# Kernel optimization log

Measured on AMD Instinct MI355X. Metric: run time of the kernel, lower is better.

## Reference

```python
import jax, jax.numpy as jnp
import numpy as np

N, D, M, K = 65536, 128, 4096, 64

def _xavier_uniform(key, shape):
    fan_out, fan_in = shape
    limit = float(np.sqrt(6.0 / (fan_in + fan_out)))
    return jax.random.uniform(key, shape, jnp.float32, -limit, limit)

def setup_inputs() -> dict:
    key = jax.random.key(0)
    kx, ke, kd = jax.random.split(key, 3)
    x = jax.random.normal(kx, (N, D), jnp.float32)
    W_enc = _xavier_uniform(ke, (M, D))          # [n_latents, input_dim]
    W_dec = _xavier_uniform(kd, (D, M))          # [input_dim, n_latents]
    # normalize decoder columns to unit norm (dim=0), clamped at 1e-8
    norms = jnp.maximum(jnp.linalg.norm(W_dec, axis=0, keepdims=True), 1e-8)
    W_dec = W_dec / norms
    b_enc = jnp.zeros((M,), jnp.float32)
    b_dec = jnp.zeros((D,), jnp.float32)
    return {"x": x, "W_enc": W_enc, "b_enc": b_enc, "W_dec": W_dec, "b_dec": b_dec}

def reference(x, W_enc, b_enc, W_dec, b_dec):
    # encode: z_pre = relu(W_enc @ (x - b_dec) + b_enc)
    z_pre = jax.nn.relu((x - b_dec) @ W_enc.T + b_enc)          # [N, M]
    # TopK activation: keep k largest, zero the rest
    vals, idx = jax.lax.top_k(z_pre, K)                          # [N, K]
    rows = jnp.arange(z_pre.shape[0])[:, None]
    z = jnp.zeros_like(z_pre).at[rows, idx].set(vals)            # sparse [N, M]
    # decode: x_hat = z @ W_dec.T + b_dec
    x_hat = z @ W_dec.T + b_dec                                  # [N, D]
    return (x_hat, z)
```

## Files before the change

kernel.cpp:

```cpp
#include <hip/hip_runtime.h>
#include <cstdint>

#define DDIM 128
#define MLAT 4096
#define KSEL 64

typedef __bf16 bf16x8 __attribute__((ext_vector_type(8)));
typedef float  f32x4  __attribute__((ext_vector_type(4)));

__global__ __launch_bounds__(256) void k_split_x(const float* __restrict__ x,
                                                 const float* __restrict__ bdec,
                                                 ushort* __restrict__ xhi,
                                                 ushort* __restrict__ xlo) {
    int e = (blockIdx.x * 256 + threadIdx.x) * 4;
    float4 v = *(const float4*)(x + e);
    float4 bd = *(const float4*)(bdec + (e & 127));
    float a[4] = {v.x - bd.x, v.y - bd.y, v.z - bd.z, v.w - bd.w};
    ushort4 h, l;
    ushort* hp = (ushort*)&h; ushort* lp = (ushort*)&l;
#pragma unroll
    for (int i = 0; i < 4; ++i) {
        unsigned ua = __float_as_uint(a[i]);
        unsigned rh = (ua + 0x7FFFu + ((ua >> 16) & 1u)) & 0xFFFF0000u;
        float lo = a[i] - __uint_as_float(rh);
        unsigned ul = __float_as_uint(lo);
        unsigned rl = ul + 0x7FFFu + ((ul >> 16) & 1u);
        hp[i] = (ushort)(rh >> 16);
        lp[i] = (ushort)(rl >> 16);
    }
    *(ushort4*)(xhi + e) = h;
    *(ushort4*)(xlo + e) = l;
}

__global__ __launch_bounds__(256) void k_split_w(const float* __restrict__ w,
                                                 ushort* __restrict__ whi,
                                                 ushort* __restrict__ wlo) {
    int e = (blockIdx.x * 256 + threadIdx.x) * 4;
    float4 v = *(const float4*)(w + e);
    float a[4] = {v.x, v.y, v.z, v.w};
    ushort4 h, l;
    ushort* hp = (ushort*)&h; ushort* lp = (ushort*)&l;
#pragma unroll
    for (int i = 0; i < 4; ++i) {
        unsigned ua = __float_as_uint(a[i]);
        unsigned rh = (ua + 0x7FFFu + ((ua >> 16) & 1u)) & 0xFFFF0000u;
        float lo = a[i] - __uint_as_float(rh);
        unsigned ul = __float_as_uint(lo);
        unsigned rl = ul + 0x7FFFu + ((ul >> 16) & 1u);
        hp[i] = (ushort)(rh >> 16);
        lp[i] = (ushort)(rl >> 16);
    }
    *(ushort4*)(whi + e) = h;
    *(ushort4*)(wlo + e) = l;
}

__global__ __launch_bounds__(256) void k_transpose(const float* __restrict__ Wdec,
                                                   float* __restrict__ WdT) {
    int tid = blockIdx.x * 256 + threadIdx.x;
    int d = tid & (DDIM - 1);
    int j = tid >> 7;
    WdT[tid] = Wdec[(size_t)d * MLAT + j];
}

__global__ __launch_bounds__(256, 2) void k_encode_mfma(
        const ushort* __restrict__ xhi, const ushort* __restrict__ xlo,
        const ushort* __restrict__ whi, const ushort* __restrict__ wlo,
        const float* __restrict__ benc, float* __restrict__ zout) {
    __shared__ __attribute__((aligned(16))) ushort Ah[128 * 128];
    __shared__ __attribute__((aligned(16))) ushort Al[128 * 128];

    const int t    = threadIdx.x;
    const int lane = t & 63;
    const int w    = t >> 6;
    const int i0   = blockIdx.x << 7;

    {
        int row = t >> 1, half = t & 1;
        const ushort* sh = xhi + (size_t)(i0 + row) * DDIM + half * 64;
        const ushort* sl = xlo + (size_t)(i0 + row) * DDIM + half * 64;
        int base = row * 256 + half * 128;
        int swz  = (row & 7) << 4;
#pragma unroll
        for (int j = 0; j < 8; ++j) {
            int off = (base + j * 16) ^ swz;
            *(bf16x8*)((char*)Ah + off) = *(const bf16x8*)(sh + j * 8);
            *(bf16x8*)((char*)Al + off) = *(const bf16x8*)(sl + j * 8);
        }
    }
    __syncthreads();

    const int lr = lane & 15;
    const int lq = lane >> 4;

    for (int cp = 0; cp < 16; ++cp) {
        const int jb = cp * 256 + (w << 6);
        f32x4 acc[8][4];
#pragma unroll
        for (int rf = 0; rf < 8; ++rf)
#pragma unroll
            for (int cf = 0; cf < 4; ++cf) acc[rf][cf] = (f32x4){0.f, 0.f, 0.f, 0.f};

        for (int ks = 0; ks < 4; ++ks) {
            bf16x8 bh[4], bl[4];
#pragma unroll
            for (int cf = 0; cf < 4; ++cf) {
                size_t boff = (size_t)(jb + cf * 16 + lr) * DDIM + ks * 32 + lq * 8;
                bh[cf] = *(const bf16x8*)(whi + boff);
                bl[cf] = *(const bf16x8*)(wlo + boff);
            }
#pragma unroll
            for (int rf = 0; rf < 8; ++rf) {
                int row = rf * 16 + lr;
                int off = (row * 256 + ks * 64 + lq * 16) ^ ((row & 7) << 4);
                bf16x8 ah = *(const bf16x8*)((const char*)Ah + off);
                bf16x8 al = *(const bf16x8*)((const char*)Al + off);
#pragma unroll
                for (int cf = 0; cf < 4; ++cf) {
                    acc[rf][cf] = __builtin_amdgcn_mfma_f32_16x16x32_bf16(ah, bh[cf], acc[rf][cf], 0, 0, 0);
                    acc[rf][cf] = __builtin_amdgcn_mfma_f32_16x16x32_bf16(ah, bl[cf], acc[rf][cf], 0, 0, 0);
                    acc[rf][cf] = __builtin_amdgcn_mfma_f32_16x16x32_bf16(al, bh[cf], acc[rf][cf], 0, 0, 0);
                }
            }
        }
#pragma unroll
        for (int rf = 0; rf < 8; ++rf)
#pragma unroll
            for (int cf = 0; cf < 4; ++cf) {
                int col = jb + cf * 16 + lr;
                float be = benc[col];
#pragma unroll
                for (int r = 0; r < 4; ++r) {
                    int row = i0 + rf * 16 + lq * 4 + r;
                    zout[(size_t)row * MLAT + col] = fmaxf(acc[rf][cf][r] + be, 0.f);
                }
            }
    }
}

__global__ __launch_bounds__(128, 8) void k_topk_decode(
        float* __restrict__ zbuf, float* __restrict__ xhat,
        const float* __restrict__ WdT, const float* __restrict__ bdec,
        const float* __restrict__ x, const float* __restrict__ Wenc,
        const float* __restrict__ benc) {
    __shared__ float sval[KSEL];
    __shared__ int   sidx[KSEL];
    __shared__ float bval[128];
    __shared__ int   bidx[128];
    __shared__ unsigned char bselm[128];
    __shared__ unsigned scom[4];
    __shared__ int stot[2];

    const int tid  = threadIdx.x;
    const int lane = tid & 63;
    const int w    = tid >> 6;
    const size_t row = blockIdx.x;
    float* zr = zbuf + row * MLAT;
    const uint4* zu = (const uint4*)zr + (w << 9);

    uint4 u[8];
#pragma unroll
    for (int q = 0; q < 8; ++q) u[q] = zu[(q << 6) + lane];

    unsigned mx = 0u;
#pragma unroll
    for (int q = 0; q < 8; ++q)
        mx = max(mx, max(max(u[q].x, u[q].y), max(u[q].z, u[q].w)));
#pragma unroll
    for (int d = 32; d >= 1; d >>= 1) mx = max(mx, (unsigned)__shfl_xor((int)mx, d, 64));
    if (lane == 0) scom[w] = mx;
    __syncthreads();
    mx = max(scom[0], scom[1]);
    __syncthreads();

#define CNT_GE(T, OUTC)                                              \
    {                                                                \
        int _c = 0;                                                  \
        _Pragma("unroll")                                            \
        for (int q = 0; q < 8; ++q) {                                \
            _c += __popcll(__ballot(u[q].x >= (T)));                 \
            _c += __popcll(__ballot(u[q].y >= (T)));                 \
            _c += __popcll(__ballot(u[q].z >= (T)));                 \
            _c += __popcll(__ballot(u[q].w >= (T)));                 \
        }                                                            \
        if (lane == 0) scom[2 + w] = (unsigned)_c;                   \
        __syncthreads();                                             \
        OUTC = (int)(scom[2] + scom[3]);                             \
        __syncthreads();                                             \
    }

    unsigned T;
    {
        unsigned hi = mx + 1u;
        unsigned lo = (mx > 0x01800000u) ? (mx - 0x01800000u) : 0u;
        int c;
        CNT_GE(lo, c);
        if (c < KSEL) { lo = 0u; c = MLAT; }
        if (c == KSEL) {
            T = lo;
        } else {
            for (;;) {
                if (hi - lo <= 1u) { T = lo; break; }
                unsigned mid = lo + ((hi - lo) >> 1);
                int cm;
                CNT_GE(mid, cm);
                if (cm == KSEL) { T = mid; break; }
                if (cm > KSEL) lo = mid; else hi = mid;
            }
        }
    }

    const float tau   = __uint_as_float(T);
    const float DELTA = 2.5e-4f;
    const float PAD   = 5.0e-5f;
    const unsigned DH = __float_as_uint(tau + DELTA + PAD);
    const unsigned DL = __float_as_uint(fmaxf(tau - DELTA, 0.f));

    unsigned inm = 0u, bandm = 0u;
#pragma unroll
    for (int q = 0; q < 8; ++q) {
        unsigned vv[4] = {u[q].x, u[q].y, u[q].z, u[q].w};
#pragma unroll
        for (int c = 0; c < 4; ++c) {
            unsigned bit = 1u << (4 * q + c);
            if (vv[c] > DH) inm |= bit;
            else if (vv[c] >= DL) bandm |= bit;
        }
    }
    {
        int packed = (__popc(inm) << 16) | __popc(bandm);
#pragma unroll
        for (int d = 32; d >= 1; d >>= 1) packed += __shfl_xor(packed, d, 64);
        if (lane == 0) scom[2 + w] = (unsigned)packed;
        __syncthreads();
    }
    int A   = (int)((scom[2] >> 16) + (scom[3] >> 16));
    int BCt = (int)((scom[2] & 0xFFFFu) + (scom[3] & 0xFFFFu));
    __syncthreads();
    int need = KSEL - A;

    unsigned sel;
    if (need <= 0) {
        sel = inm;
    } else if (BCt == need) {
        sel = inm | bandm;
    } else {
        int BC2 = min(BCt, 128);
        int bc = __popc(bandm);
        int pre = bc;
#pragma unroll
        for (int d = 1; d < 64; d <<= 1) {
            int y = __shfl_up(pre, d, 64);
            if (lane >= d) pre += y;
        }
        int wtot = __shfl(pre, 63, 64);
        if (lane == 0) stot[w] = wtot;
        __syncthreads();
        int sbase = (pre - bc) + (w ? stot[0] : 0);
        {
            unsigned mm = bandm; int o = 0;
            while (mm) {
                int bp = __ffs(mm) - 1; mm &= mm - 1;
                int slot = sbase + o; ++o;
                if (slot < 128)
                    bidx[slot] = (w << 11) + ((bp >> 2) << 8) + (lane << 2) + (bp & 3);
            }
        }
        __syncthreads();
        for (int s = tid; s < BC2; s += 128) {
            int j = bidx[s];
            const float* wr = Wenc + (size_t)j * DDIM;
            const float* xr = x + row * DDIM;
            float a = 0.f;
            for (int k = 0; k < DDIM; ++k) a = fmaf(xr[k] - bdec[k], wr[k], a);
            bval[s] = fmaxf(a + benc[j], 0.f);
        }
        __syncthreads();
        if (tid == 0) {
            for (int s = 0; s < BC2; ++s) bselm[s] = 0;
            int take = min(need, BC2);
            for (int it = 0; it < take; ++it) {
                float bv = -1.f; int bi = 0x7FFFFFFF, bs = 0;
                for (int s = 0; s < BC2; ++s) {
                    if (bselm[s]) continue;
                    float v = bval[s]; int j = bidx[s];
                    if (v > bv || (v == bv && j < bi)) { bv = v; bi = j; bs = s; }
                }
                bselm[bs] = 1;
            }
        }
        __syncthreads();
        sel = inm;
        {
            unsigned mm = bandm; int o = 0;
            while (mm) {
                int bp = __ffs(mm) - 1; mm &= mm - 1;
                int slot = sbase + o; ++o;
                if (slot < 128 && bselm[slot]) sel |= 1u << bp;
            }
        }
        __syncthreads();
    }

    int scnt = __popc(sel);
    int pre = scnt;
#pragma unroll
    for (int d = 1; d < 64; d <<= 1) {
        int y = __shfl_up(pre, d, 64);
        if (lane >= d) pre += y;
    }
    int wtot2 = __shfl(pre, 63, 64);
    if (lane == 0) stot[w] = wtot2;
    __syncthreads();
    int pos = pre - scnt + (w ? stot[0] : 0);
    int total = stot[0] + stot[1];

    uint4* zw = (uint4*)zr + (w << 9);
#pragma unroll
    for (int q = 0; q < 8; ++q) {
        uint4 o;
        bool s0 = (sel >> (4 * q + 0)) & 1u;
        bool s1 = (sel >> (4 * q + 1)) & 1u;
        bool s2 = (sel >> (4 * q + 2)) & 1u;
        bool s3 = (sel >> (4 * q + 3)) & 1u;
        o.x = s0 ? u[q].x : 0u;
        o.y = s1 ? u[q].y : 0u;
        o.z = s2 ? u[q].z : 0u;
        o.w = s3 ? u[q].w : 0u;
        int base = (w << 11) + (q << 8) + (lane << 2);
        if (s0 && pos < KSEL) { sval[pos] = __uint_as_float(u[q].x); sidx[pos] = base + 0; ++pos; }
        if (s1 && pos < KSEL) { sval[pos] = __uint_as_float(u[q].y); sidx[pos] = base + 1; ++pos; }
        if (s2 && pos < KSEL) { sval[pos] = __uint_as_float(u[q].z); sidx[pos] = base + 2; ++pos; }
        if (s3 && pos < KSEL) { sval[pos] = __uint_as_float(u[q].w); sidx[pos] = base + 3; ++pos; }
        zw[(q << 6) + lane] = o;
    }
    __syncthreads();

    float a = bdec[tid];
    int tt = min(total, KSEL);
#pragma unroll 4
    for (int s = 0; s < tt; ++s) {
        float v = sval[s];
        int   j = sidx[s];
        a = fmaf(v, WdT[(size_t)j * DDIM + tid], a);
    }
    xhat[row * DDIM + tid] = a;
}

extern "C" void kernel_launch(void* const* d_in, const int* in_sizes, int n_in,
                              void* d_out, int out_size, void* d_ws, size_t ws_size,
                              hipStream_t stream) {
    const float* x    = (const float*)d_in[0];
    const float* Wenc = (const float*)d_in[1];
    const float* benc = (const float*)d_in[2];
    const float* Wdec = (const float*)d_in[3];
    const float* bdec = (const float*)d_in[4];

    const int N = in_sizes[0] / DDIM;
    float* xhat = (float*)d_out;
    float* zbuf = (float*)d_out + (size_t)N * DDIM;

    ushort* xhi = (ushort*)d_out;
    ushort* xlo = xhi + (size_t)N * DDIM;

    ushort* whi = (ushort*)d_ws;
    ushort* wlo = whi + (size_t)MLAT * DDIM;
    float*  WdT = (float*)((char*)d_ws + 2u * 1024u * 1024u);

    k_split_x<<<dim3((N * DDIM) / 1024), dim3(256), 0, stream>>>(x, bdec, xhi, xlo);
    k_split_w<<<dim3((MLAT * DDIM) / 1024), dim3(256), 0, stream>>>(Wenc, whi, wlo);
    k_transpose<<<dim3((MLAT * DDIM) / 256), dim3(256), 0, stream>>>(Wdec, WdT);
    k_encode_mfma<<<dim3(N / 128), dim3(256), 0, stream>>>(xhi, xlo, whi, wlo, benc, zbuf);
    k_topk_decode<<<dim3(N), dim3(128), 0, stream>>>(zbuf, xhat, WdT, bdec, x, Wenc, benc);
}
```

Baseline: 888.7 us.

## Store encoder output as bf16 and recompute selected latents exactly in topk

The encoder now writes pre-activations as bf16 codes to a workspace buffer instead of fp32 into the output, which halves that write and the read that follows. The topk/decode kernel selects candidates on the bf16 values using a relative tolerance band. It then recomputes the chosen latents and borderline entries in fp32 from x and W_enc, and writes the dense fp32 z itself. The three prep kernels are merged into one launch, and W_enc is prepacked into an MFMA-friendly layout so B-fragment loads are contiguous and can be prefetched one k-step ahead. The risk is mis-selection if the band is too narrow, plus extra per-row dot products for the recomputation.

```diff
diff --git a/kernel.cpp b/kernel.cpp
--- a/kernel.cpp
+++ b/kernel.cpp
@@ -8,64 +8,65 @@
 typedef __bf16 bf16x8 __attribute__((ext_vector_type(8)));
 typedef float  f32x4  __attribute__((ext_vector_type(4)));
 
-__global__ __launch_bounds__(256) void k_split_x(const float* __restrict__ x,
-                                                 const float* __restrict__ bdec,
-                                                 ushort* __restrict__ xhi,
-                                                 ushort* __restrict__ xlo) {
-    int e = (blockIdx.x * 256 + threadIdx.x) * 4;
-    float4 v = *(const float4*)(x + e);
-    float4 bd = *(const float4*)(bdec + (e & 127));
-    float a[4] = {v.x - bd.x, v.y - bd.y, v.z - bd.z, v.w - bd.w};
-    ushort4 h, l;
-    ushort* hp = (ushort*)&h; ushort* lp = (ushort*)&l;
-#pragma unroll
-    for (int i = 0; i < 4; ++i) {
-        unsigned ua = __float_as_uint(a[i]);
-        unsigned rh = (ua + 0x7FFFu + ((ua >> 16) & 1u)) & 0xFFFF0000u;
-        float lo = a[i] - __uint_as_float(rh);
-        unsigned ul = __float_as_uint(lo);
-        unsigned rl = ul + 0x7FFFu + ((ul >> 16) & 1u);
-        hp[i] = (ushort)(rh >> 16);
-        lp[i] = (ushort)(rl >> 16);
-    }
-    *(ushort4*)(xhi + e) = h;
-    *(ushort4*)(xlo + e) = l;
+__device__ __forceinline__ ushort bf16rn(float v) {
+    unsigned b = __float_as_uint(v);
+    return (ushort)((b + 0x7FFFu + ((b >> 16) & 1u)) >> 16);
 }
 
-__global__ __launch_bounds__(256) void k_split_w(const float* __restrict__ w,
-                                                 ushort* __restrict__ whi,
-                                                 ushort* __restrict__ wlo) {
-    int e = (blockIdx.x * 256 + threadIdx.x) * 4;
-    float4 v = *(const float4*)(w + e);
-    float a[4] = {v.x, v.y, v.z, v.w};
-    ushort4 h, l;
-    ushort* hp = (ushort*)&h; ushort* lp = (ushort*)&l;
-#pragma unroll
-    for (int i = 0; i < 4; ++i) {
-        unsigned ua = __float_as_uint(a[i]);
-        unsigned rh = (ua + 0x7FFFu + ((ua >> 16) & 1u)) & 0xFFFF0000u;
-        float lo = a[i] - __uint_as_float(rh);
-        unsigned ul = __float_as_uint(lo);
-        unsigned rl = ul + 0x7FFFu + ((ul >> 16) & 1u);
-        hp[i] = (ushort)(rh >> 16);
-        lp[i] = (ushort)(rl >> 16);
-    }
-    *(ushort4*)(whi + e) = h;
-    *(ushort4*)(wlo + e) = l;
-}
-
-__global__ __launch_bounds__(256) void k_transpose(const float* __restrict__ Wdec,
-                                                   float* __restrict__ WdT) {
-    int tid = blockIdx.x * 256 + threadIdx.x;
-    int d = tid & (DDIM - 1);
-    int j = tid >> 7;
-    WdT[tid] = Wdec[(size_t)d * MLAT + j];
+__global__ __launch_bounds__(256) void k_prep(
+        const float* __restrict__ x, const float* __restrict__ bdec,
+        ushort* __restrict__ xhi, ushort* __restrict__ xlo,
+        const float* __restrict__ Wenc,
+        ushort* __restrict__ whiP, ushort* __restrict__ wloP,
+        const float* __restrict__ Wdec, float* __restrict__ WdT) {
+    int b = blockIdx.x;
+    if (b < 8192) {
+        int e = (b * 256 + threadIdx.x) * 4;
+        float4 v = *(const float4*)(x + e);
+        float4 bd = *(const float4*)(bdec + (e & 127));
+        float a[4] = {v.x - bd.x, v.y - bd.y, v.z - bd.z, v.w - bd.w};
+        ushort4 h, l;
+        ushort* hp = (ushort*)&h; ushort* lp = (ushort*)&l;
+#pragma unroll
+        for (int i = 0; i < 4; ++i) {
+            unsigned ua = __float_as_uint(a[i]);
+            unsigned rh = (ua + 0x7FFFu + ((ua >> 16) & 1u)) & 0xFFFF0000u;
+            float lo = a[i] - __uint_as_float(rh);
+            hp[i] = (ushort)(rh >> 16);
+            lp[i] = bf16rn(lo);
+        }
+        *(ushort4*)(xhi + e) = h;
+        *(ushort4*)(xlo + e) = l;
+    } else if (b < 8704) {
+        int e = ((b - 8192) * 256 + threadIdx.x) * 4;
+        float4 v = *(const float4*)(Wenc + e);
+        float a[4] = {v.x, v.y, v.z, v.w};
+        int c = e >> 7, k0 = e & 127;
+        int ks = k0 >> 5, lq = (k0 >> 3) & 3, j0 = k0 & 7;
+        int out = (((c >> 4) * 4 + ks) * 4 + lq) * 128 + (c & 15) * 8 + j0;
+        ushort4 h, l;
+        ushort* hp = (ushort*)&h; ushort* lp = (ushort*)&l;
+#pragma unroll
+        for (int i = 0; i < 4; ++i) {
+            unsigned ua = __float_as_uint(a[i]);
+            unsigned rh = (ua + 0x7FFFu + ((ua >> 16) & 1u)) & 0xFFFF0000u;
+            float lo = a[i] - __uint_as_float(rh);
+            hp[i] = (ushort)(rh >> 16);
+            lp[i] = bf16rn(lo);
+        }
+        *(ushort4*)(whiP + out) = h;
+        *(ushort4*)(wloP + out) = l;
+    } else {
+        int tid = (b - 8704) * 256 + threadIdx.x;
+        int d = tid >> 12, j = tid & 4095;
+        WdT[j * DDIM + d] = Wdec[tid];
+    }
 }
 
 __global__ __launch_bounds__(256, 2) void k_encode_mfma(
         const ushort* __restrict__ xhi, const ushort* __restrict__ xlo,
-        const ushort* __restrict__ whi, const ushort* __restrict__ wlo,
-        const float* __restrict__ benc, float* __restrict__ zout) {
+        const ushort* __restrict__ whiP, const ushort* __restrict__ wloP,
+        const float* __restrict__ benc, ushort* __restrict__ zt) {
     __shared__ __attribute__((aligned(16))) ushort Ah[128 * 128];
     __shared__ __attribute__((aligned(16))) ushort Al[128 * 128];
 
@@ -94,19 +95,29 @@
 
     for (int cp = 0; cp < 16; ++cp) {
         const int jb = cp * 256 + (w << 6);
+        const int tb = jb >> 4;
         f32x4 acc[8][4];
 #pragma unroll
         for (int rf = 0; rf < 8; ++rf)
 #pragma unroll
             for (int cf = 0; cf < 4; ++cf) acc[rf][cf] = (f32x4){0.f, 0.f, 0.f, 0.f};
 
+#define BOFF(cf, ks) ((size_t)((((tb + (cf)) << 2) + (ks)) << 9) + (lane << 3))
+        bf16x8 bhc[4], blc[4];
+#pragma unroll
+        for (int cf = 0; cf < 4; ++cf) {
+            bhc[cf] = *(const bf16x8*)(whiP + BOFF(cf, 0));
+            blc[cf] = *(const bf16x8*)(wloP + BOFF(cf, 0));
+        }
+#pragma unroll
         for (int ks = 0; ks < 4; ++ks) {
-            bf16x8 bh[4], bl[4];
-#pragma unroll
-            for (int cf = 0; cf < 4; ++cf) {
-                size_t boff = (size_t)(jb + cf * 16 + lr) * DDIM + ks * 32 + lq * 8;
-                bh[cf] = *(const bf16x8*)(whi + boff);
-                bl[cf] = *(const bf16x8*)(wlo + boff);
+            bf16x8 bhn[4], bln[4];
+            if (ks < 3) {
+#pragma unroll
+                for (int cf = 0; cf < 4; ++cf) {
+                    bhn[cf] = *(const bf16x8*)(whiP + BOFF(cf, ks + 1));
+                    bln[cf] = *(const bf16x8*)(wloP + BOFF(cf, ks + 1));
+                }
             }
 #pragma unroll
             for (int rf = 0; rf < 8; ++rf) {
@@ -116,12 +127,17 @@
                 bf16x8 al = *(const bf16x8*)((const char*)Al + off);
 #pragma unroll
                 for (int cf = 0; cf < 4; ++cf) {
-                    acc[rf][cf] = __builtin_amdgcn_mfma_f32_16x16x32_bf16(ah, bh[cf], acc[rf][cf], 0, 0, 0);
-                    acc[rf][cf] = __builtin_amdgcn_mfma_f32_16x16x32_bf16(ah, bl[cf], acc[rf][cf], 0, 0, 0);
-                    acc[rf][cf] = __builtin_amdgcn_mfma_f32_16x16x32_bf16(al, bh[cf], acc[rf][cf], 0, 0, 0);
+                    acc[rf][cf] = __builtin_amdgcn_mfma_f32_16x16x32_bf16(ah, bhc[cf], acc[rf][cf], 0, 0, 0);
+                    acc[rf][cf] = __builtin_amdgcn_mfma_f32_16x16x32_bf16(ah, blc[cf], acc[rf][cf], 0, 0, 0);
+                    acc[rf][cf] = __builtin_amdgcn_mfma_f32_16x16x32_bf16(al, bhc[cf], acc[rf][cf], 0, 0, 0);
                 }
             }
-        }
+            if (ks < 3) {
+#pragma unroll
+                for (int cf = 0; cf < 4; ++cf) { bhc[cf] = bhn[cf]; blc[cf] = bln[cf]; }
+            }
+        }
+#undef BOFF
 #pragma unroll
         for (int rf = 0; rf < 8; ++rf)
 #pragma unroll
@@ -131,22 +147,24 @@
 #pragma unroll
                 for (int r = 0; r < 4; ++r) {
                     int row = i0 + rf * 16 + lq * 4 + r;
-                    zout[(size_t)row * MLAT + col] = fmaxf(acc[rf][cf][r] + be, 0.f);
+                    zt[(size_t)row * MLAT + col] = bf16rn(fmaxf(acc[rf][cf][r] + be, 0.f));
                 }
             }
     }
 }
 
 __global__ __launch_bounds__(128, 8) void k_topk_decode(
-        float* __restrict__ zbuf, float* __restrict__ xhat,
+        const ushort* __restrict__ zt, float* __restrict__ zout,
+        float* __restrict__ xhat,
         const float* __restrict__ WdT, const float* __restrict__ bdec,
         const float* __restrict__ x, const float* __restrict__ Wenc,
         const float* __restrict__ benc) {
+    __shared__ float xmb[DDIM];
     __shared__ float sval[KSEL];
     __shared__ int   sidx[KSEL];
-    __shared__ float bval[128];
-    __shared__ int   bidx[128];
-    __shared__ unsigned char bselm[128];
+    __shared__ float bval[256];
+    __shared__ int   bidx[256];
+    __shared__ unsigned char bselm[256];
     __shared__ unsigned scom[4];
     __shared__ int stot[2];
 
@@ -154,17 +172,21 @@
     const int lane = tid & 63;
     const int w    = tid >> 6;
     const size_t row = blockIdx.x;
-    float* zr = zbuf + row * MLAT;
-    const uint4* zu = (const uint4*)zr + (w << 9);
-
-    uint4 u[8];
-#pragma unroll
-    for (int q = 0; q < 8; ++q) u[q] = zu[(q << 6) + lane];
+
+    xmb[tid] = x[row * DDIM + tid] - bdec[tid];
+
+    const uint4* zr = (const uint4*)(zt + row * MLAT) + (w << 8);
+    uint4 u[4];
+#pragma unroll
+    for (int q = 0; q < 4; ++q) u[q] = zr[(q << 6) + lane];
 
     unsigned mx = 0u;
 #pragma unroll
-    for (int q = 0; q < 8; ++q)
-        mx = max(mx, max(max(u[q].x, u[q].y), max(u[q].z, u[q].w)));
+    for (int q = 0; q < 4; ++q) {
+        unsigned r0 = u[q].x, r1 = u[q].y, r2 = u[q].z, r3 = u[q].w;
+        mx = max(mx, max(max(r0 & 0xFFFFu, r0 >> 16), max(r1 & 0xFFFFu, r1 >> 16)));
+        mx = max(mx, max(max(r2 & 0xFFFFu, r2 >> 16), max(r3 & 0xFFFFu, r3 >> 16)));
+    }
 #pragma unroll
     for (int d = 32; d >= 1; d >>= 1) mx = max(mx, (unsigned)__shfl_xor((int)mx, d, 64));
     if (lane == 0) scom[w] = mx;
@@ -172,26 +194,30 @@
     mx = max(scom[0], scom[1]);
     __syncthreads();
 
-#define CNT_GE(T, OUTC)                                              \
-    {                                                                \
-        int _c = 0;                                                  \
-        _Pragma("unroll")                                            \
-        for (int q = 0; q < 8; ++q) {                                \
-            _c += __popcll(__ballot(u[q].x >= (T)));                 \
-            _c += __popcll(__ballot(u[q].y >= (T)));                 \
-            _c += __popcll(__ballot(u[q].z >= (T)));                 \
-            _c += __popcll(__ballot(u[q].w >= (T)));                 \
-        }                                                            \
-        if (lane == 0) scom[2 + w] = (unsigned)_c;                   \
-        __syncthreads();                                             \
-        OUTC = (int)(scom[2] + scom[3]);                             \
-        __syncthreads();                                             \
+#define CNT_GE(T, OUTC)                                                    \
+    {                                                                      \
+        int _c = 0;                                                        \
+        _Pragma("unroll")                                                  \
+        for (int q = 0; q < 4; ++q) {                                      \
+            _c += __popcll(__ballot((u[q].x & 0xFFFFu) >= (T)));           \
+            _c += __popcll(__ballot((u[q].x >> 16)     >= (T)));           \
+            _c += __popcll(__ballot((u[q].y & 0xFFFFu) >= (T)));           \
+            _c += __popcll(__ballot((u[q].y >> 16)     >= (T)));           \
+            _c += __popcll(__ballot((u[q].z & 0xFFFFu) >= (T)));           \
+            _c += __popcll(__ballot((u[q].z >> 16)     >= (T)));           \
+            _c += __popcll(__ballot((u[q].w & 0xFFFFu) >= (T)));           \
+            _c += __popcll(__ballot((u[q].w >> 16)     >= (T)));           \
+        }                                                                  \
+        if (lane == 0) scom[2 + w] = (unsigned)_c;                         \
+        __syncthreads();                                                   \
+        OUTC = (int)(scom[2] + scom[3]);                                   \
+        __syncthreads();                                                   \
     }
 
     unsigned T;
     {
         unsigned hi = mx + 1u;
-        unsigned lo = (mx > 0x01800000u) ? (mx - 0x01800000u) : 0u;
+        unsigned lo = (mx > 384u) ? (mx - 384u) : 0u;
         int c;
         CNT_GE(lo, c);
         if (c < KSEL) { lo = 0u; c = MLAT; }
@@ -209,21 +235,25 @@
         }
     }
 
-    const float tau   = __uint_as_float(T);
-    const float DELTA = 2.5e-4f;
-    const float PAD   = 5.0e-5f;
-    const unsigned DH = __float_as_uint(tau + DELTA + PAD);
-    const unsigned DL = __float_as_uint(fmaxf(tau - DELTA, 0.f));
+    const float tauf  = __uint_as_float(T << 16);
+    const float DELTA = tauf * 0.01f + 2.0e-4f;
+    const float DH = tauf + DELTA;
+    const float DL = tauf - DELTA;
 
     unsigned inm = 0u, bandm = 0u;
 #pragma unroll
-    for (int q = 0; q < 8; ++q) {
-        unsigned vv[4] = {u[q].x, u[q].y, u[q].z, u[q].w};
-#pragma unroll
-        for (int c = 0; c < 4; ++c) {
-            unsigned bit = 1u << (4 * q + c);
-            if (vv[c] > DH) inm |= bit;
-            else if (vv[c] >= DL) bandm |= bit;
+    for (int q = 0; q < 4; ++q) {
+        unsigned rr[4] = {u[q].x, u[q].y, u[q].z, u[q].w};
+#pragma unroll
+        for (int ri = 0; ri < 4; ++ri) {
+#pragma unroll
+            for (int hb = 0; hb < 2; ++hb) {
+                unsigned code = hb ? (rr[ri] >> 16) : (rr[ri] & 0xFFFFu);
+                float f = __uint_as_float(code << 16);
+                unsigned bit = 1u << (q * 8 + ri * 2 + hb);
+                if (f > DH) inm |= bit;
+                else if (f >= DL) bandm |= bit;
+            }
         }
     }
     {
@@ -233,18 +263,13 @@
         if (lane == 0) scom[2 + w] = (unsigned)packed;
         __syncthreads();
     }
-    int A   = (int)((scom[2] >> 16) + (scom[3] >> 16));
-    int BCt = (int)((scom[2] & 0xFFFFu) + (scom[3] & 0xFFFFu));
-    __syncthreads();
-    int need = KSEL - A;
-
-    unsigned sel;
-    if (need <= 0) {
-        sel = inm;
-    } else if (BCt == need) {
-        sel = inm | bandm;
-    } else {
-        int BC2 = min(BCt, 128);
+    const int A   = (int)((scom[2] >> 16) + (scom[3] >> 16));
+    const int BCt = (int)((scom[2] & 0xFFFFu) + (scom[3] & 0xFFFFu));
+    __syncthreads();
+    const int need = KSEL - A;
+    const int BC2 = min(BCt, 256);
+
+    {
         int bc = __popc(bandm);
         int pre = bc;
 #pragma unroll
@@ -254,29 +279,26 @@
         }
         int wtot = __shfl(pre, 63, 64);
         if (lane == 0) stot[w] = wtot;
+        for (int s = tid; s < 256; s += 128) bselm[s] = 0;
         __syncthreads();
         int sbase = (pre - bc) + (w ? stot[0] : 0);
-        {
-            unsigned mm = bandm; int o = 0;
-            while (mm) {
-                int bp = __ffs(mm) - 1; mm &= mm - 1;
-                int slot = sbase + o; ++o;
-                if (slot < 128)
-                    bidx[slot] = (w << 11) + ((bp >> 2) << 8) + (lane << 2) + (bp & 3);
-            }
+        unsigned mm = bandm; int o = 0;
+        while (mm) {
+            int bp = __ffs(mm) - 1; mm &= mm - 1;
+            int slot = sbase + o; ++o;
+            if (slot < 256)
+                bidx[slot] = (w << 11) + ((bp >> 3) << 9) + (lane << 3) + (bp & 7);
         }
         __syncthreads();
         for (int s = tid; s < BC2; s += 128) {
             int j = bidx[s];
             const float* wr = Wenc + (size_t)j * DDIM;
-            const float* xr = x + row * DDIM;
             float a = 0.f;
-            for (int k = 0; k < DDIM; ++k) a = fmaf(xr[k] - bdec[k], wr[k], a);
+            for (int k = 0; k < DDIM; ++k) a = fmaf(xmb[k], wr[k], a);
             bval[s] = fmaxf(a + benc[j], 0.f);
         }
         __syncthreads();
         if (tid == 0) {
-            for (int s = 0; s < BC2; ++s) bselm[s] = 0;
             int take = min(need, BC2);
             for (int it = 0; it < take; ++it) {
                 float bv = -1.f; int bi = 0x7FFFFFFF, bs = 0;
@@ -289,17 +311,16 @@
             }
         }
         __syncthreads();
-        sel = inm;
-        {
-            unsigned mm = bandm; int o = 0;
-            while (mm) {
-                int bp = __ffs(mm) - 1; mm &= mm - 1;
-                int slot = sbase + o; ++o;
-                if (slot < 128 && bselm[slot]) sel |= 1u << bp;
-            }
-        }
-        __syncthreads();
-    }
+        mm = bandm; o = 0;
+        unsigned selb = 0u;
+        while (mm) {
+            int bp = __ffs(mm) - 1; mm &= mm - 1;
+            int slot = sbase + o; ++o;
+            if (slot < 256 && bselm[slot]) selb |= 1u << bp;
+        }
+        bandm = selb;
+    }
+    const unsigned sel = inm | bandm;
 
     int scnt = __popc(sel);
     int pre = scnt;
@@ -309,40 +330,59 @@
         if (lane >= d) pre += y;
     }
     int wtot2 = __shfl(pre, 63, 64);
+    __syncthreads();
     if (lane == 0) stot[w] = wtot2;
     __syncthreads();
-    int pos = pre - scnt + (w ? stot[0] : 0);
-    int total = stot[0] + stot[1];
-
-    uint4* zw = (uint4*)zr + (w << 9);
-#pragma unroll
-    for (int q = 0; q < 8; ++q) {
-        uint4 o;
-        bool s0 = (sel >> (4 * q + 0)) & 1u;
-        bool s1 = (sel >> (4 * q + 1)) & 1u;
-        bool s2 = (sel >> (4 * q + 2)) & 1u;
-        bool s3 = (sel >> (4 * q + 3)) & 1u;
-        o.x = s0 ? u[q].x : 0u;
-        o.y = s1 ? u[q].y : 0u;
-        o.z = s2 ? u[q].z : 0u;
-        o.w = s3 ? u[q].w : 0u;
-        int base = (w << 11) + (q << 8) + (lane << 2);
-        if (s0 && pos < KSEL) { sval[pos] = __uint_as_float(u[q].x); sidx[pos] = base + 0; ++pos; }
-        if (s1 && pos < KSEL) { sval[pos] = __uint_as_float(u[q].y); sidx[pos] = base + 1; ++pos; }
-        if (s2 && pos < KSEL) { sval[pos] = __uint_as_float(u[q].z); sidx[pos] = base + 2; ++pos; }
-        if (s3 && pos < KSEL) { sval[pos] = __uint_as_float(u[q].w); sidx[pos] = base + 3; ++pos; }
-        zw[(q << 6) + lane] = o;
-    }
-    __syncthreads();
+    const int pos0 = pre - scnt + (w ? stot[0] : 0);
+    const int total = min(stot[0] + stot[1], KSEL);
+
+    {
+        int pos = pos0;
+#pragma unroll
+        for (int q = 0; q < 4; ++q) {
+#pragma unroll
+            for (int h = 0; h < 8; ++h) {
+                if ((sel >> (q * 8 + h)) & 1u) {
+                    if (pos < KSEL)
+                        sidx[pos] = (w << 11) + (q << 9) + (lane << 3) + h;
+                    ++pos;
+                }
+            }
+        }
+    }
+    __syncthreads();
+
+    for (int s = tid; s < total; s += 128) {
+        int j = sidx[s];
+        const float* wr = Wenc + (size_t)j * DDIM;
+        float a = 0.f;
+        for (int k = 0; k < DDIM; ++k) a = fmaf(xmb[k], wr[k], a);
+        sval[s] = fmaxf(a + benc[j], 0.f);
+    }
+    __syncthreads();
+
+    {
+        float* zo = zout + row * MLAT + (w << 11);
+        int pos = pos0;
+#pragma unroll
+        for (int q = 0; q < 4; ++q) {
+            float o[8];
+#pragma unroll
+            for (int h = 0; h < 8; ++h) {
+                bool s = (sel >> (q * 8 + h)) & 1u;
+                o[h] = (s && pos < KSEL) ? sval[pos] : 0.f;
+                pos += s ? 1 : 0;
+            }
+            float* dst = zo + (q << 9) + (lane << 3);
+            *(float4*)(dst)     = (float4){o[0], o[1], o[2], o[3]};
+            *(float4*)(dst + 4) = (float4){o[4], o[5], o[6], o[7]};
+        }
+    }
 
     float a = bdec[tid];
-    int tt = min(total, KSEL);
 #pragma unroll 4
-    for (int s = 0; s < tt; ++s) {
-        float v = sval[s];
-        int   j = sidx[s];
-        a = fmaf(v, WdT[(size_t)j * DDIM + tid], a);
-    }
+    for (int s = 0; s < total; ++s)
+        a = fmaf(sval[s], WdT[(size_t)sidx[s] * DDIM + tid], a);
     xhat[row * DDIM + tid] = a;
 }
 
@@ -357,18 +397,20 @@
 
     const int N = in_sizes[0] / DDIM;
     float* xhat = (float*)d_out;
-    float* zbuf = (float*)d_out + (size_t)N * DDIM;
+    float* zout = (float*)d_out + (size_t)N * DDIM;
 
     ushort* xhi = (ushort*)d_out;
     ushort* xlo = xhi + (size_t)N * DDIM;
 
-    ushort* whi = (ushort*)d_ws;
-    ushort* wlo = whi + (size_t)MLAT * DDIM;
-    float*  WdT = (float*)((char*)d_ws + 2u * 1024u * 1024u);
-
-    k_split_x<<<dim3((N * DDIM) / 1024), dim3(256), 0, stream>>>(x, bdec, xhi, xlo);
-    k_split_w<<<dim3((MLAT * DDIM) / 1024), dim3(256), 0, stream>>>(Wenc, whi, wlo);
-    k_transpose<<<dim3((MLAT * DDIM) / 256), dim3(256), 0, stream>>>(Wdec, WdT);
-    k_encode_mfma<<<dim3(N / 128), dim3(256), 0, stream>>>(xhi, xlo, whi, wlo, benc, zbuf);
-    k_topk_decode<<<dim3(N), dim3(128), 0, stream>>>(zbuf, xhat, WdT, bdec, x, Wenc, benc);
+    ushort* whiP = (ushort*)d_ws;
+    ushort* wloP = whiP + (size_t)MLAT * DDIM;
+    float*  WdT  = (float*)((char*)d_ws + 2u * 1024u * 1024u);
+    ushort* zt   = (ushort*)((char*)d_ws + 4u * 1024u * 1024u);
+
+    k_prep<<<dim3(8192 + 512 + 2048), dim3(256), 0, stream>>>(
+        x, bdec, xhi, xlo, Wenc, whiP, wloP, Wdec, WdT);
+    k_encode_mfma<<<dim3(N / 128), dim3(256), 0, stream>>>(
+        xhi, xlo, whiP, wloP, benc, zt);
+    k_topk_decode<<<dim3(N), dim3(128), 0, stream>>>(
+        zt, zout, xhat, WdT, bdec, x, Wenc, benc);
 }
```

After: 1.647 ms. 85.3% more time.

## Fuse prep kernels, prepack encoder weights in MFMA fragment order, prefetch B fragments

Applied to the files above, without the earlier changes.

Merges the three preprocessing kernels into one launch, with block ranges selecting x split, W_enc split or W_dec transpose. The W_enc hi/lo halves are now stored in MFMA-fragment order, so each lane's B-operand load becomes one contiguous 16-byte read per lane instead of a row-strided gather. The encode loop double-buffers B fragments, loading step ks+1 while step ks runs its MFMAs. The aim is to cut launch overhead and global-load latency in the encode GEMM, at the cost of more registers in a kernel already bounded at 2 blocks per CU.

```diff
diff --git a/kernel.cpp b/kernel.cpp
--- a/kernel.cpp
+++ b/kernel.cpp
@@ -8,63 +8,64 @@
 typedef __bf16 bf16x8 __attribute__((ext_vector_type(8)));
 typedef float  f32x4  __attribute__((ext_vector_type(4)));
 
-__global__ __launch_bounds__(256) void k_split_x(const float* __restrict__ x,
-                                                 const float* __restrict__ bdec,
-                                                 ushort* __restrict__ xhi,
-                                                 ushort* __restrict__ xlo) {
-    int e = (blockIdx.x * 256 + threadIdx.x) * 4;
-    float4 v = *(const float4*)(x + e);
-    float4 bd = *(const float4*)(bdec + (e & 127));
-    float a[4] = {v.x - bd.x, v.y - bd.y, v.z - bd.z, v.w - bd.w};
-    ushort4 h, l;
-    ushort* hp = (ushort*)&h; ushort* lp = (ushort*)&l;
-#pragma unroll
-    for (int i = 0; i < 4; ++i) {
-        unsigned ua = __float_as_uint(a[i]);
-        unsigned rh = (ua + 0x7FFFu + ((ua >> 16) & 1u)) & 0xFFFF0000u;
-        float lo = a[i] - __uint_as_float(rh);
-        unsigned ul = __float_as_uint(lo);
-        unsigned rl = ul + 0x7FFFu + ((ul >> 16) & 1u);
-        hp[i] = (ushort)(rh >> 16);
-        lp[i] = (ushort)(rl >> 16);
-    }
-    *(ushort4*)(xhi + e) = h;
-    *(ushort4*)(xlo + e) = l;
-}
-
-__global__ __launch_bounds__(256) void k_split_w(const float* __restrict__ w,
-                                                 ushort* __restrict__ whi,
-                                                 ushort* __restrict__ wlo) {
-    int e = (blockIdx.x * 256 + threadIdx.x) * 4;
-    float4 v = *(const float4*)(w + e);
-    float a[4] = {v.x, v.y, v.z, v.w};
-    ushort4 h, l;
-    ushort* hp = (ushort*)&h; ushort* lp = (ushort*)&l;
-#pragma unroll
-    for (int i = 0; i < 4; ++i) {
-        unsigned ua = __float_as_uint(a[i]);
-        unsigned rh = (ua + 0x7FFFu + ((ua >> 16) & 1u)) & 0xFFFF0000u;
-        float lo = a[i] - __uint_as_float(rh);
-        unsigned ul = __float_as_uint(lo);
-        unsigned rl = ul + 0x7FFFu + ((ul >> 16) & 1u);
-        hp[i] = (ushort)(rh >> 16);
-        lp[i] = (ushort)(rl >> 16);
-    }
-    *(ushort4*)(whi + e) = h;
-    *(ushort4*)(wlo + e) = l;
-}
-
-__global__ __launch_bounds__(256) void k_transpose(const float* __restrict__ Wdec,
-                                                   float* __restrict__ WdT) {
-    int tid = blockIdx.x * 256 + threadIdx.x;
-    int d = tid & (DDIM - 1);
-    int j = tid >> 7;
-    WdT[tid] = Wdec[(size_t)d * MLAT + j];
+__device__ __forceinline__ ushort bf16rn(float v) {
+    unsigned b = __float_as_uint(v);
+    return (ushort)((b + 0x7FFFu + ((b >> 16) & 1u)) >> 16);
+}
+
+__global__ __launch_bounds__(256) void k_prep(
+        const float* __restrict__ x, const float* __restrict__ bdec,
+        ushort* __restrict__ xhi, ushort* __restrict__ xlo,
+        const float* __restrict__ Wenc,
+        ushort* __restrict__ whiP, ushort* __restrict__ wloP,
+        const float* __restrict__ Wdec, float* __restrict__ WdT) {
+    int b = blockIdx.x;
+    if (b < 8192) {
+        int e = (b * 256 + threadIdx.x) * 4;
+        float4 v = *(const float4*)(x + e);
+        float4 bd = *(const float4*)(bdec + (e & 127));
+        float a[4] = {v.x - bd.x, v.y - bd.y, v.z - bd.z, v.w - bd.w};
+        ushort4 h, l;
+        ushort* hp = (ushort*)&h; ushort* lp = (ushort*)&l;
+#pragma unroll
+        for (int i = 0; i < 4; ++i) {
+            unsigned ua = __float_as_uint(a[i]);
+            unsigned rh = (ua + 0x7FFFu + ((ua >> 16) & 1u)) & 0xFFFF0000u;
+            float lo = a[i] - __uint_as_float(rh);
+            hp[i] = (ushort)(rh >> 16);
+            lp[i] = bf16rn(lo);
+        }
+        *(ushort4*)(xhi + e) = h;
+        *(ushort4*)(xlo + e) = l;
+    } else if (b < 8704) {
+        int e = ((b - 8192) * 256 + threadIdx.x) * 4;
+        float4 v = *(const float4*)(Wenc + e);
+        float a[4] = {v.x, v.y, v.z, v.w};
+        int c = e >> 7, k0 = e & 127;
+        int ks = k0 >> 5, lq = (k0 >> 3) & 3, j0 = k0 & 7;
+        int out = (((c >> 4) * 4 + ks) * 4 + lq) * 128 + (c & 15) * 8 + j0;
+        ushort4 h, l;
+        ushort* hp = (ushort*)&h; ushort* lp = (ushort*)&l;
+#pragma unroll
+        for (int i = 0; i < 4; ++i) {
+            unsigned ua = __float_as_uint(a[i]);
+            unsigned rh = (ua + 0x7FFFu + ((ua >> 16) & 1u)) & 0xFFFF0000u;
+            float lo = a[i] - __uint_as_float(rh);
+            hp[i] = (ushort)(rh >> 16);
+            lp[i] = bf16rn(lo);
+        }
+        *(ushort4*)(whiP + out) = h;
+        *(ushort4*)(wloP + out) = l;
+    } else {
+        int tid = (b - 8704) * 256 + threadIdx.x;
+        int d = tid >> 12, j = tid & 4095;
+        WdT[j * DDIM + d] = Wdec[tid];
+    }
 }
 
 __global__ __launch_bounds__(256, 2) void k_encode_mfma(
         const ushort* __restrict__ xhi, const ushort* __restrict__ xlo,
-        const ushort* __restrict__ whi, const ushort* __restrict__ wlo,
+        const ushort* __restrict__ whiP, const ushort* __restrict__ wloP,
         const float* __restrict__ benc, float* __restrict__ zout) {
     __shared__ __attribute__((aligned(16))) ushort Ah[128 * 128];
     __shared__ __attribute__((aligned(16))) ushort Al[128 * 128];
@@ -94,19 +95,29 @@
 
     for (int cp = 0; cp < 16; ++cp) {
         const int jb = cp * 256 + (w << 6);
+        const int tb = jb >> 4;
         f32x4 acc[8][4];
 #pragma unroll
         for (int rf = 0; rf < 8; ++rf)
 #pragma unroll
             for (int cf = 0; cf < 4; ++cf) acc[rf][cf] = (f32x4){0.f, 0.f, 0.f, 0.f};
 
+#define BOFF(cf, ks) ((size_t)((((tb + (cf)) << 2) + (ks)) << 9) + (lane << 3))
+        bf16x8 bhc[4], blc[4];
+#pragma unroll
+        for (int cf = 0; cf < 4; ++cf) {
+            bhc[cf] = *(const bf16x8*)(whiP + BOFF(cf, 0));
+            blc[cf] = *(const bf16x8*)(wloP + BOFF(cf, 0));
+        }
+#pragma unroll
         for (int ks = 0; ks < 4; ++ks) {
-            bf16x8 bh[4], bl[4];
-#pragma unroll
-            for (int cf = 0; cf < 4; ++cf) {
-                size_t boff = (size_t)(jb + cf * 16 + lr) * DDIM + ks * 32 + lq * 8;
-                bh[cf] = *(const bf16x8*)(whi + boff);
-                bl[cf] = *(const bf16x8*)(wlo + boff);
+            bf16x8 bhn[4], bln[4];
+            if (ks < 3) {
+#pragma unroll
+                for (int cf = 0; cf < 4; ++cf) {
+                    bhn[cf] = *(const bf16x8*)(whiP + BOFF(cf, ks + 1));
+                    bln[cf] = *(const bf16x8*)(wloP + BOFF(cf, ks + 1));
+                }
             }
 #pragma unroll
             for (int rf = 0; rf < 8; ++rf) {
@@ -116,12 +127,17 @@
                 bf16x8 al = *(const bf16x8*)((const char*)Al + off);
 #pragma unroll
                 for (int cf = 0; cf < 4; ++cf) {
-                    acc[rf][cf] = __builtin_amdgcn_mfma_f32_16x16x32_bf16(ah, bh[cf], acc[rf][cf], 0, 0, 0);
-                    acc[rf][cf] = __builtin_amdgcn_mfma_f32_16x16x32_bf16(ah, bl[cf], acc[rf][cf], 0, 0, 0);
-                    acc[rf][cf] = __builtin_amdgcn_mfma_f32_16x16x32_bf16(al, bh[cf], acc[rf][cf], 0, 0, 0);
+                    acc[rf][cf] = __builtin_amdgcn_mfma_f32_16x16x32_bf16(ah, bhc[cf], acc[rf][cf], 0, 0, 0);
+                    acc[rf][cf] = __builtin_amdgcn_mfma_f32_16x16x32_bf16(ah, blc[cf], acc[rf][cf], 0, 0, 0);
+                    acc[rf][cf] = __builtin_amdgcn_mfma_f32_16x16x32_bf16(al, bhc[cf], acc[rf][cf], 0, 0, 0);
                 }
             }
-        }
+            if (ks < 3) {
+#pragma unroll
+                for (int cf = 0; cf < 4; ++cf) { bhc[cf] = bhn[cf]; blc[cf] = bln[cf]; }
+            }
+        }
+#undef BOFF
 #pragma unroll
         for (int rf = 0; rf < 8; ++rf)
 #pragma unroll
@@ -362,13 +378,14 @@
     ushort* xhi = (ushort*)d_out;
     ushort* xlo = xhi + (size_t)N * DDIM;
 
-    ushort* whi = (ushort*)d_ws;
-    ushort* wlo = whi + (size_t)MLAT * DDIM;
-    float*  WdT = (float*)((char*)d_ws + 2u * 1024u * 1024u);
-
-    k_split_x<<<dim3((N * DDIM) / 1024), dim3(256), 0, stream>>>(x, bdec, xhi, xlo);
-    k_split_w<<<dim3((MLAT * DDIM) / 1024), dim3(256), 0, stream>>>(Wenc, whi, wlo);
-    k_transpose<<<dim3((MLAT * DDIM) / 256), dim3(256), 0, stream>>>(Wdec, WdT);
-    k_encode_mfma<<<dim3(N / 128), dim3(256), 0, stream>>>(xhi, xlo, whi, wlo, benc, zbuf);
-    k_topk_decode<<<dim3(N), dim3(128), 0, stream>>>(zbuf, xhat, WdT, bdec, x, Wenc, benc);
-}
+    ushort* whiP = (ushort*)d_ws;
+    ushort* wloP = whiP + (size_t)MLAT * DDIM;
+    float*  WdT  = (float*)((char*)d_ws + 2u * 1024u * 1024u);
+
+    k_prep<<<dim3(8192 + 512 + 2048), dim3(256), 0, stream>>>(
+        x, bdec, xhi, xlo, Wenc, whiP, wloP, Wdec, WdT);
+    k_encode_mfma<<<dim3(N / 128), dim3(256), 0, stream>>>(
+        xhi, xlo, whiP, wloP, benc, zbuf);
+    k_topk_decode<<<dim3(N), dim3(128), 0, stream>>>(
+        zbuf, xhat, WdT, bdec, x, Wenc, benc);
+}
```

After: 842.8 us. 5.2% less time.
